# Kernel optimization log

Hardware: AMD Instinct MI355X
Metric: run time of the kernel (lower is better)

## Reference

```python
import jax, jax.numpy as jnp
import numpy as np
from jax.ops import segment_sum

N_NODE, N_EDGE, D_IN, D_HID, N_CLS = 50000, 800000, 64, 64, 40


def setup_inputs() -> dict:
    key = jax.random.key(0)
    k1, k2, k3, k4 = jax.random.split(key, 4)
    x = jax.random.normal(k1, (N_NODE, D_IN), dtype=jnp.float32)
    edge_index = jax.random.randint(k2, (2, N_EDGE), 0, N_NODE, dtype=jnp.int64)
    W1 = jax.random.normal(k3, (D_IN, D_HID), dtype=jnp.float32) * (1.0 / np.sqrt(D_IN))
    b1 = jnp.zeros((D_HID,), dtype=jnp.float32)
    W2 = jax.random.normal(k4, (D_HID, N_CLS), dtype=jnp.float32) * (1.0 / np.sqrt(D_HID))
    b2 = jnp.zeros((N_CLS,), dtype=jnp.float32)
    return {"x": x, "edge_index": edge_index, "W1": W1, "b1": b1, "W2": W2, "b2": b2}


def _att_weights(fea, row, col, n):
    # edge-parallel cosine similarity (sklearn cosine_similarity restricted to edges)
    nrm = jnp.sqrt(jnp.sum(fea * fea, axis=1, keepdims=True))
    fn = fea / jnp.maximum(nrm, 1e-12)
    sim = jnp.sum(fn[row] * fn[col], axis=1)                 # [E]
    sim = jnp.where(sim < 0.1, 0.0, sim)                      # threshold
    # L1 row-normalization (sim >= 0 after threshold)
    rs = segment_sum(sim, row, num_segments=n)                # [N]
    sim_n = jnp.where(sim > 0, sim / jnp.maximum(rs[row], 1e-12), 0.0)
    # degree-based self-loop weight lam = 1/(deg+1)
    deg = segment_sum((sim > 0).astype(fea.dtype), row, num_segments=n)
    lam = 1.0 / (deg + 1.0)
    # exp applied only to stored (nonzero) entries; zeroed edges stay 0
    w_edge = jnp.where(sim > 0, jnp.exp(sim_n), 0.0)          # [E]
    w_self = jnp.exp(lam)                                     # [N] self-loop weights
    return w_edge, w_self


def _gcn(h, W, b, row, col, w_edge, w_self, n):
    # symmetric-norm GCN over weighted edges + explicit self loops
    deg = segment_sum(w_edge, row, num_segments=n) + w_self
    dinv = 1.0 / jnp.sqrt(jnp.maximum(deg, 1e-12))
    h = h @ W                                                 # [N, F]
    coef = w_edge * dinv[row] * dinv[col]                     # [E]
    out = segment_sum(coef[:, None] * h[col], row, num_segments=n)
    out = out + (w_self * dinv * dinv)[:, None] * h + b
    return out


def reference(x, edge_index, W1, b1, W2, b2):
    n = x.shape[0]
    row, col = edge_index[0], edge_index[1]
    # layer 1: attention coefs from raw features
    w1e, w1s = _att_weights(x, row, col, n)
    h = jax.nn.relu(_gcn(x, W1, b1, row, col, w1e, w1s, n))
    # layer 2: attention coefs recomputed on hidden features (dropout = eval mode)
    w2e, w2s = _att_weights(h, row, col, n)
    out = _gcn(h, W2, b2, row, col, w2e, w2s, n)
    return jax.nn.log_softmax(out, axis=1)
```

## Files before the change

kernel.cpp:

```cpp
#include <hip/hip_runtime.h>
#include <math.h>


#define ATT_CAP 96
#define EPB     2048
#define RPB     128
#define NBUCK_MAX 512
#define CAPB    4096

typedef _Float16 half4 __attribute__((ext_vector_type(4)));

__global__ void k_normfn(const float* __restrict__ fea, float* __restrict__ fn, int n)
{
    int gid  = blockIdx.x * blockDim.x + threadIdx.x;
    int wid  = gid >> 6;
    int lane = threadIdx.x & 63;
    if (wid >= n) return;
    float v = fea[(size_t)wid * 64 + lane];
    float s = v * v;
#pragma unroll
    for (int off = 32; off > 0; off >>= 1) s += __shfl_xor(s, off);
    float inv = 1.0f / fmaxf(sqrtf(s), 1e-12f);
    fn[(size_t)wid * 64 + lane] = v * inv;
}

__global__ void k_bscat(const int* __restrict__ row, const int* __restrict__ col,
                        int* __restrict__ gcur, int* __restrict__ ebuf, int E, int nbuck)
{
    __shared__ int lh[NBUCK_MAX];
    __shared__ int lbase[NBUCK_MAX];
    int b = blockIdx.x;
    int ebeg = b * EPB;
    int rr[8], cc[8];
    for (int i = threadIdx.x; i < nbuck; i += blockDim.x) lh[i] = 0;
    __syncthreads();
#pragma unroll
    for (int k = 0; k < 8; ++k) {
        int e = ebeg + k * 256 + threadIdx.x;
        bool v = (e < E);
        int r = v ? row[e] : -1;
        int c = v ? col[e] : 0;
        rr[k] = r; cc[k] = c;
        if (v) atomicAdd(&lh[r >> 7], 1);
    }
    __syncthreads();
    for (int i = threadIdx.x; i < nbuck; i += blockDim.x) {
        int cnt = lh[i];
        if (cnt) lbase[i] = i * CAPB + atomicAdd(gcur + i, cnt);
        lh[i] = 0;
    }
    __syncthreads();
#pragma unroll
    for (int k = 0; k < 8; ++k) {
        int r = rr[k];
        if (r >= 0) {
            int j = r >> 7;
            int pos = lbase[j] + atomicAdd(&lh[j], 1);
            ebuf[pos] = ((r & (RPB - 1)) << 16) | cc[k];
        }
    }
}

__global__ void k_csr(const int* __restrict__ ebuf, const int* __restrict__ gcur,
                      int* __restrict__ rptr, int* __restrict__ col_s,
                      int N, int E, int nbuck)
{
    __shared__ int pk[CAPB];
    __shared__ int lcol[CAPB];
    __shared__ int lcnt[RPB], lexc[RPB], lcur[RPB];
    __shared__ int spart[4];
    int j = blockIdx.x;
    int tid = threadIdx.x;
    int lane = tid & 63, wave = tid >> 6;

    int part = 0;
    for (int i = tid; i < j; i += blockDim.x) part += gcur[i];
#pragma unroll
    for (int off = 32; off > 0; off >>= 1) part += __shfl_xor(part, off);
    if (lane == 0) spart[wave] = part;
    if (tid < RPB) lcnt[tid] = 0;
    __syncthreads();
    int beg = spart[0] + spart[1] + spart[2] + spart[3];
    int m = gcur[j]; if (m > CAPB) m = CAPB;

    const int* seg = ebuf + (size_t)j * CAPB;
    for (int i = tid; i < m; i += blockDim.x) pk[i] = seg[i];
    __syncthreads();
    for (int i = tid; i < m; i += blockDim.x) atomicAdd(&lcnt[pk[i] >> 16], 1);
    __syncthreads();
    if (tid < 64) {
        int a = lcnt[2 * tid], b2 = lcnt[2 * tid + 1];
        int s = a + b2;
        int incl = s;
#pragma unroll
        for (int off = 1; off < 64; off <<= 1) {
            int v = __shfl_up(incl, off);
            if (tid >= off) incl += v;
        }
        int base = incl - s;
        lexc[2 * tid] = base;     lexc[2 * tid + 1] = base + a;
        lcur[2 * tid] = base;     lcur[2 * tid + 1] = base + a;
    }
    __syncthreads();
    for (int i = tid; i < m; i += blockDim.x) {
        int v = pk[i];
        int p = atomicAdd(&lcur[v >> 16], 1);
        lcol[p] = v & 0xFFFF;
    }
    __syncthreads();
    for (int i = tid; i < m; i += blockDim.x) col_s[beg + i] = lcol[i];
    if (tid < RPB) {
        int r = j * RPB + tid;
        if (r < N) rptr[r] = beg + lexc[tid];
    }
    if (j == 0 && tid == 0) rptr[N] = E;
}

__global__ void k_att(const float* __restrict__ fn,
                      const int* __restrict__ rptr, const int* __restrict__ col_s,
                      int2* __restrict__ cw, int* __restrict__ lend,
                      float* __restrict__ dinv, float* __restrict__ selfc, int n)
{
    __shared__ float ssim[4][ATT_CAP];
    __shared__ int   scol[4][ATT_CAP];
    int wib  = threadIdx.x >> 6;
    int wid  = blockIdx.x * 4 + wib;
    int lane = threadIdx.x & 63;
    if (wid >= n) return;
    int sub = lane & 3;
    int grp = lane >> 2;
    int beg = rptr[wid], end = rptr[wid + 1];
    int deg_all = end - beg;

    const float4* frp = (const float4*)(fn + (size_t)wid * 64);
    float4 a0 = frp[sub], a1 = frp[sub + 4], a2 = frp[sub + 8], a3 = frp[sub + 12];

    float rs_part = 0.0f;
    int ngrp = (deg_all + 15) >> 4;
    for (int g = 0; g < ngrp; ++g) {
        int li = g * 16 + grp;
        float s = 0.0f; int c = 0;
        bool valid = (li < deg_all);
        if (valid) {
            c = col_s[beg + li];
            const float4* fcp = (const float4*)(fn + (size_t)c * 64);
            float4 b0 = fcp[sub], b1 = fcp[sub + 4], b2 = fcp[sub + 8], b3 = fcp[sub + 12];
            float p = a0.x * b0.x + a0.y * b0.y + a0.z * b0.z + a0.w * b0.w
                    + a1.x * b1.x + a1.y * b1.y + a1.z * b1.z + a1.w * b1.w
                    + a2.x * b2.x + a2.y * b2.y + a2.z * b2.z + a2.w * b2.w
                    + a3.x * b3.x + a3.y * b3.y + a3.z * b3.z + a3.w * b3.w;
            p += __shfl_xor(p, 1);
            p += __shfl_xor(p, 2);
            s = (p < 0.1f) ? 0.0f : p;
        }
        if (sub == 0 && valid) {
            if (li < ATT_CAP) { ssim[wib][li] = s; scol[wib][li] = c; }
            if (s > 0.0f) rs_part += s;
        }
    }
#pragma unroll
    for (int off = 32; off > 0; off >>= 1) rs_part += __shfl_xor(rs_part, off);
    float denom = fmaxf(rs_part, 1e-12f);

    int   nlive = 0;
    float sw_lane = 0.0f;
    for (int base = 0; base < deg_all; base += 64) {
        int li = base + lane;
        bool valid = (li < deg_all);
        float s = 0.0f; int c = 0;
        if (valid) {
            if (li < ATT_CAP) { s = ssim[wib][li]; c = scol[wib][li]; }
            else {
                c = col_s[beg + li];
                const float* fr = fn + (size_t)wid * 64;
                const float* fc = fn + (size_t)c * 64;
                float p = 0.0f;
                for (int k = 0; k < 64; ++k) p += fr[k] * fc[k];
                s = (p < 0.1f) ? 0.0f : p;
            }
        }
        float w = (valid && s > 0.0f) ? expf(s / denom) : 0.0f;
        unsigned long long M = __ballot(w > 0.0f);
        int rank = __popcll(M & ((1ull << lane) - 1ull));
        if (w > 0.0f) {
            int2 pw; pw.x = c; pw.y = __float_as_int(w);
            cw[beg + nlive + rank] = pw;
            sw_lane += w;
        }
        nlive += __popcll(M);
    }
#pragma unroll
    for (int off = 32; off > 0; off >>= 1) sw_lane += __shfl_xor(sw_lane, off);

    if (lane == 0) {
        float wself = expf(1.0f / ((float)nlive + 1.0f));
        float D  = sw_lane + wself;
        float di = rsqrtf(fmaxf(D, 1e-12f));
        lend[wid]  = beg + nlive;
        dinv[wid]  = di;
        selfc[wid] = wself * di;
    }
}

template <int F, typename InT, typename OutT>
__global__ void k_gemm(const InT* __restrict__ fea, const float* __restrict__ W,
                       const float* __restrict__ scale, OutT* __restrict__ out, int n)
{
    constexpr int R = 256 / F;
    __shared__ float sW[64 * F];
    __shared__ float sX[R * 64];
    int tid = threadIdx.x;
    for (int i = tid; i < 64 * F; i += 256) sW[i] = W[i];
    int base = blockIdx.x * R;
    for (int i = tid; i < R * 64; i += 256) {
        int rr = base + i / 64;
        sX[i] = (rr < n) ? (float)fea[(size_t)rr * 64 + (i & 63)] : 0.0f;
    }
    __syncthreads();
    int rl = tid / F, j = tid % F;
    if (rl >= R) return;
    int r = base + rl;
    if (r >= n) return;
    float acc = 0.0f;
#pragma unroll
    for (int k = 0; k < 64; ++k) acc = fmaf(sX[rl * 64 + k], sW[k * F + j], acc);
    out[(size_t)r * F + j] = (OutT)(acc * scale[r]);
}

template <int F, typename Vec4>
__device__ inline float agg_core_t(const Vec4* __restrict__ hdv,
                                   const int2* __restrict__ cw,
                                   int beg, int lend_, int lane)
{
    int q  = lane & 15;
    int eg = lane >> 4;
    bool qact = (F == 64) ? true : (q < (F >> 2));
    float acc0 = 0.f, acc1 = 0.f, acc2 = 0.f, acc3 = 0.f;
    for (int base = beg; base < lend_; base += 64) {
        int idx = base + lane;
        int cv = 0; float wv = 0.0f;
        if (idx < lend_) { int2 pw = cw[idx]; cv = pw.x; wv = __int_as_float(pw.y); }
        int cnt = lend_ - base; if (cnt > 64) cnt = 64;
        for (int j = 0; j < cnt; j += 4) {
            int   c = __shfl(cv, j + eg);
            float w = __shfl(wv, j + eg);
            if (qact) {
                Vec4 hv = hdv[(size_t)c * (F >> 2) + q];
                acc0 += w * (float)hv.x;
                acc1 += w * (float)hv.y;
                acc2 += w * (float)hv.z;
                acc3 += w * (float)hv.w;
            }
        }
    }
    acc0 += __shfl_xor(acc0, 16); acc0 += __shfl_xor(acc0, 32);
    acc1 += __shfl_xor(acc1, 16); acc1 += __shfl_xor(acc1, 32);
    acc2 += __shfl_xor(acc2, 16); acc2 += __shfl_xor(acc2, 32);
    acc3 += __shfl_xor(acc3, 16); acc3 += __shfl_xor(acc3, 32);
    int srcq = lane >> 2;
    float a0 = __shfl(acc0, srcq);
    float a1 = __shfl(acc1, srcq);
    float a2 = __shfl(acc2, srcq);
    float a3 = __shfl(acc3, srcq);
    int k = lane & 3;
    return (k == 0) ? a0 : (k == 1) ? a1 : (k == 2) ? a2 : a3;
}

__global__ void k_agg64(const float* __restrict__ hd, const int2* __restrict__ cw,
                        const float* __restrict__ dinv, const float* __restrict__ selfc,
                        const float* __restrict__ b, const int* __restrict__ row_ptr,
                        const int* __restrict__ lend,
                        _Float16* __restrict__ hrelu16, float* __restrict__ fnh, int n)
{
    int gid  = blockIdx.x * blockDim.x + threadIdx.x;
    int wid  = gid >> 6;
    int lane = threadIdx.x & 63;
    if (wid >= n) return;
    int beg = row_ptr[wid], le = lend[wid];
    float accf = agg_core_t<64>((const float4*)hd, cw, beg, le, lane);
    float hs  = hd[(size_t)wid * 64 + lane];
    float v = dinv[wid] * accf + selfc[wid] * hs + b[lane];
    v = fmaxf(v, 0.0f);
    hrelu16[(size_t)wid * 64 + lane] = (_Float16)v;
    float s = v * v;
#pragma unroll
    for (int off = 32; off > 0; off >>= 1) s += __shfl_xor(s, off);
    float inv = 1.0f / fmaxf(sqrtf(s), 1e-12f);
    fnh[(size_t)wid * 64 + lane] = v * inv;
}

__global__ void k_agg40_lsm(const _Float16* __restrict__ hd2, const int2* __restrict__ cw,
                            const float* __restrict__ dinv, const float* __restrict__ selfc,
                            const float* __restrict__ b, const int* __restrict__ row_ptr,
                            const int* __restrict__ lend,
                            float* __restrict__ out, int n)
{
    constexpr int F = 40;
    int gid  = blockIdx.x * blockDim.x + threadIdx.x;
    int wid  = gid >> 6;
    int lane = threadIdx.x & 63;
    if (wid >= n) return;
    int beg = row_ptr[wid], le = lend[wid];
    float accf = agg_core_t<F>((const half4*)hd2, cw, beg, le, lane);
    bool active = (lane < F);
    float v = 0.0f;
    if (active) {
        float hs = (float)hd2[(size_t)wid * F + lane];
        v = dinv[wid] * accf + selfc[wid] * hs + b[lane];
    }
    float m = active ? v : -__builtin_inff();
#pragma unroll
    for (int off = 32; off > 0; off >>= 1) m = fmaxf(m, __shfl_xor(m, off));
    float ex = active ? expf(v - m) : 0.0f;
    float s = ex;
#pragma unroll
    for (int off = 32; off > 0; off >>= 1) s += __shfl_xor(s, off);
    if (active) out[(size_t)wid * F + lane] = v - m - logf(s);
}

extern "C" void kernel_launch(void* const* d_in, const int* in_sizes, int n_in,
                              void* d_out, int out_size, void* d_ws, size_t ws_size,
                              hipStream_t stream)
{
    const float* x  = (const float*)d_in[0];
    const int*   ei = (const int*)d_in[1];
    const float* W1 = (const float*)d_in[2];
    const float* b1 = (const float*)d_in[3];
    const float* W2 = (const float*)d_in[4];
    const float* b2 = (const float*)d_in[5];
    float* out = (float*)d_out;

    const int N = in_sizes[0] / 64;
    const int E = in_sizes[1] / 2;
    const int* row = ei;
    const int* col = ei + E;

    const int nblkA = (E + EPB - 1) / EPB;
    const int nbuck = (N + RPB - 1) / RPB;

    char* p = (char*)d_ws;
    auto alloc = [&](size_t bytes) -> char* {
        char* r = p; p += (bytes + 255) & ~(size_t)255; return r;
    };
    float*     fn     = (float*)alloc((size_t)N * 64 * 4);
    float*     dinv   = (float*)alloc((size_t)N * 4);
    float*     selfc  = (float*)alloc((size_t)N * 4);
    float*     hd1    = (float*)alloc((size_t)N * 64 * 4);
    _Float16*  hrelu  = (_Float16*)alloc((size_t)N * 64 * 2);
    _Float16*  hd2    = (_Float16*)alloc((size_t)N * 40 * 2);
    float*     fnh    = (float*)alloc((size_t)N * 64 * 4);
    int*       rptr   = (int*)alloc((size_t)(N + 1) * 4);
    int*       lendv  = (int*)alloc((size_t)N * 4);
    int*       col_s  = (int*)alloc((size_t)E * 4);
    int2*      cw     = (int2*)alloc((size_t)E * 8);
    int*       ebuf   = (int*)alloc((size_t)nbuck * CAPB * 4);
    int*       gcur   = (int*)alloc((size_t)nbuck * 4);

    const int TB = 256;
    int blk_nodeWave = (N * 64 + TB - 1) / TB;
    int blk_node4    = (N + 3) / 4;

    hipMemsetAsync(gcur, 0, (size_t)nbuck * 4, stream);

    k_bscat<<<nblkA, TB, 0, stream>>>(row, col, gcur, ebuf, E, nbuck);
    k_csr<<<nbuck, TB, 0, stream>>>(ebuf, gcur, rptr, col_s, N, E, nbuck);

    k_normfn<<<blk_nodeWave, TB, 0, stream>>>(x, fn, N);
    k_att<<<blk_node4, TB, 0, stream>>>(fn, rptr, col_s, cw, lendv, dinv, selfc, N);
    k_gemm<64, float, float><<<(N + 3) / 4, TB, 0, stream>>>(x, W1, dinv, hd1, N);
    k_agg64<<<blk_nodeWave, TB, 0, stream>>>(hd1, cw, dinv, selfc, b1,
                                             rptr, lendv, hrelu, fnh, N);

    k_att<<<blk_node4, TB, 0, stream>>>(fnh, rptr, col_s, cw, lendv, dinv, selfc, N);
    k_gemm<40, _Float16, _Float16><<<(N + 5) / 6, TB, 0, stream>>>(hrelu, W2, dinv, hd2, N);
    k_agg40_lsm<<<blk_nodeWave, TB, 0, stream>>>(hd2, cw, dinv, selfc, b2,
                                                 rptr, lendv, out, N);
}
```

Measured before the change: 268.4 us.

## Fuse norm into bucket scatter and layer-2 GEMM into aggregation/attention

The feature-normalization kernel now runs as extra blocks in the bucket-scatter launch, saving one kernel launch. The layer-2 dense projection is computed per node inside k_agg64 from W2 held in shared memory, written as fp32 g2. The second k_att pass then scales it by dinv and emits the fp16 hd2, which removes the separate GEMM kernel and the fp16 hrelu round trip. In exchange, k_agg64 gains a 10 KB shared W2 load per block and a serial 64-step dot product per lane, and adds an fp32 g2 buffer write and read.

```diff
diff --git a/kernel.cpp b/kernel.cpp
--- a/kernel.cpp
+++ b/kernel.cpp
@@ -10,25 +10,26 @@
 
 typedef _Float16 half4 __attribute__((ext_vector_type(4)));
 
-__global__ void k_normfn(const float* __restrict__ fea, float* __restrict__ fn, int n)
-{
-    int gid  = blockIdx.x * blockDim.x + threadIdx.x;
-    int wid  = gid >> 6;
-    int lane = threadIdx.x & 63;
-    if (wid >= n) return;
-    float v = fea[(size_t)wid * 64 + lane];
-    float s = v * v;
-#pragma unroll
-    for (int off = 32; off > 0; off >>= 1) s += __shfl_xor(s, off);
-    float inv = 1.0f / fmaxf(sqrtf(s), 1e-12f);
-    fn[(size_t)wid * 64 + lane] = v * inv;
-}
-
-__global__ void k_bscat(const int* __restrict__ row, const int* __restrict__ col,
-                        int* __restrict__ gcur, int* __restrict__ ebuf, int E, int nbuck)
+__global__ void k_bscat_norm(const int* __restrict__ row, const int* __restrict__ col,
+                             int* __restrict__ gcur, int* __restrict__ ebuf,
+                             int E, int nbuck, int nblkA,
+                             const float* __restrict__ x, float* __restrict__ fn, int N)
 {
     __shared__ int lh[NBUCK_MAX];
     __shared__ int lbase[NBUCK_MAX];
+    if ((int)blockIdx.x >= nblkA) {
+        int gid  = (blockIdx.x - nblkA) * blockDim.x + threadIdx.x;
+        int wid  = gid >> 6;
+        int lane = threadIdx.x & 63;
+        if (wid >= N) return;
+        float v = x[(size_t)wid * 64 + lane];
+        float s = v * v;
+#pragma unroll
+        for (int off = 32; off > 0; off >>= 1) s += __shfl_xor(s, off);
+        float inv = 1.0f / fmaxf(sqrtf(s), 1e-12f);
+        fn[(size_t)wid * 64 + lane] = v * inv;
+        return;
+    }
     int b = blockIdx.x;
     int ebeg = b * EPB;
     int rr[8], cc[8];
@@ -119,7 +120,8 @@
 __global__ void k_att(const float* __restrict__ fn,
                       const int* __restrict__ rptr, const int* __restrict__ col_s,
                       int2* __restrict__ cw, int* __restrict__ lend,
-                      float* __restrict__ dinv, float* __restrict__ selfc, int n)
+                      float* __restrict__ dinv, float* __restrict__ selfc,
+                      const float* __restrict__ g2, _Float16* __restrict__ hd2, int n)
 {
     __shared__ float ssim[4][ATT_CAP];
     __shared__ int   scol[4][ATT_CAP];
@@ -192,14 +194,16 @@
 #pragma unroll
     for (int off = 32; off > 0; off >>= 1) sw_lane += __shfl_xor(sw_lane, off);
 
+    float wself = expf(1.0f / ((float)nlive + 1.0f));
+    float D  = sw_lane + wself;
+    float di = rsqrtf(fmaxf(D, 1e-12f));
     if (lane == 0) {
-        float wself = expf(1.0f / ((float)nlive + 1.0f));
-        float D  = sw_lane + wself;
-        float di = rsqrtf(fmaxf(D, 1e-12f));
         lend[wid]  = beg + nlive;
         dinv[wid]  = di;
         selfc[wid] = wself * di;
     }
+    if (g2 && lane < 40)
+        hd2[(size_t)wid * 40 + lane] = (_Float16)(g2[(size_t)wid * 40 + lane] * di);
 }
 
 template <int F, typename InT, typename OutT>
@@ -269,24 +273,38 @@
 __global__ void k_agg64(const float* __restrict__ hd, const int2* __restrict__ cw,
                         const float* __restrict__ dinv, const float* __restrict__ selfc,
                         const float* __restrict__ b, const int* __restrict__ row_ptr,
-                        const int* __restrict__ lend,
-                        _Float16* __restrict__ hrelu16, float* __restrict__ fnh, int n)
-{
-    int gid  = blockIdx.x * blockDim.x + threadIdx.x;
+                        const int* __restrict__ lend, const float* __restrict__ W2,
+                        float* __restrict__ g2, float* __restrict__ fnh, int n)
+{
+    __shared__ float sW2[64 * 40];
+    __shared__ float sv[4][64];
+    int tid = threadIdx.x;
+    for (int i = tid; i < 64 * 40; i += 256) sW2[i] = W2[i];
+    __syncthreads();
+
+    int gid  = blockIdx.x * blockDim.x + tid;
     int wid  = gid >> 6;
-    int lane = threadIdx.x & 63;
+    int lane = tid & 63;
+    int wib  = tid >> 6;
     if (wid >= n) return;
     int beg = row_ptr[wid], le = lend[wid];
     float accf = agg_core_t<64>((const float4*)hd, cw, beg, le, lane);
     float hs  = hd[(size_t)wid * 64 + lane];
     float v = dinv[wid] * accf + selfc[wid] * hs + b[lane];
     v = fmaxf(v, 0.0f);
-    hrelu16[(size_t)wid * 64 + lane] = (_Float16)v;
     float s = v * v;
 #pragma unroll
     for (int off = 32; off > 0; off >>= 1) s += __shfl_xor(s, off);
     float inv = 1.0f / fmaxf(sqrtf(s), 1e-12f);
     fnh[(size_t)wid * 64 + lane] = v * inv;
+
+    sv[wib][lane] = v;
+    if (lane < 40) {
+        float acc = 0.0f;
+#pragma unroll
+        for (int k = 0; k < 64; ++k) acc = fmaf(sv[wib][k], sW2[k * 40 + lane], acc);
+        g2[(size_t)wid * 40 + lane] = acc;
+    }
 }
 
 __global__ void k_agg40_lsm(const _Float16* __restrict__ hd2, const int2* __restrict__ cw,
@@ -346,7 +364,7 @@
     float*     dinv   = (float*)alloc((size_t)N * 4);
     float*     selfc  = (float*)alloc((size_t)N * 4);
     float*     hd1    = (float*)alloc((size_t)N * 64 * 4);
-    _Float16*  hrelu  = (_Float16*)alloc((size_t)N * 64 * 2);
+    float*     g2     = (float*)alloc((size_t)N * 40 * 4);
     _Float16*  hd2    = (_Float16*)alloc((size_t)N * 40 * 2);
     float*     fnh    = (float*)alloc((size_t)N * 64 * 4);
     int*       rptr   = (int*)alloc((size_t)(N + 1) * 4);
@@ -362,17 +380,18 @@
 
     hipMemsetAsync(gcur, 0, (size_t)nbuck * 4, stream);
 
-    k_bscat<<<nblkA, TB, 0, stream>>>(row, col, gcur, ebuf, E, nbuck);
+    k_bscat_norm<<<nblkA + blk_nodeWave, TB, 0, stream>>>(row, col, gcur, ebuf,
+                                                          E, nbuck, nblkA, x, fn, N);
     k_csr<<<nbuck, TB, 0, stream>>>(ebuf, gcur, rptr, col_s, N, E, nbuck);
 
-    k_normfn<<<blk_nodeWave, TB, 0, stream>>>(x, fn, N);
-    k_att<<<blk_node4, TB, 0, stream>>>(fn, rptr, col_s, cw, lendv, dinv, selfc, N);
+    k_att<<<blk_node4, TB, 0, stream>>>(fn, rptr, col_s, cw, lendv, dinv, selfc,
+                                        (const float*)nullptr, (_Float16*)nullptr, N);
     k_gemm<64, float, float><<<(N + 3) / 4, TB, 0, stream>>>(x, W1, dinv, hd1, N);
     k_agg64<<<blk_nodeWave, TB, 0, stream>>>(hd1, cw, dinv, selfc, b1,
-                                             rptr, lendv, hrelu, fnh, N);
-
-    k_att<<<blk_node4, TB, 0, stream>>>(fnh, rptr, col_s, cw, lendv, dinv, selfc, N);
-    k_gemm<40, _Float16, _Float16><<<(N + 5) / 6, TB, 0, stream>>>(hrelu, W2, dinv, hd2, N);
+                                             rptr, lendv, W2, g2, fnh, N);
+
+    k_att<<<blk_node4, TB, 0, stream>>>(fnh, rptr, col_s, cw, lendv, dinv, selfc,
+                                        g2, hd2, N);
     k_agg40_lsm<<<blk_nodeWave, TB, 0, stream>>>(hd2, cw, dinv, selfc, b2,
                                                  rptr, lendv, out, N);
 }
```

Result: faster. 262.3 us (-2.2%).
